# Kernel optimization log

Measured on AMD Instinct MI355X. Metric: run time of the kernel, lower is better.

Reference implementation:

```python
import jax, jax.numpy as jnp
import numpy as np

B, S, D, H, HD = 2, 4096, 1024, 16, 64   # batch, seq, hidden, heads, head_dim
BLOCK, W = 64, 8                          # block size, local window in blocks (512 tokens)
ROPE_BASE = 10000.0


def _rope_tables(seq_len, dim, dtype):
    inv_freq = 1.0 / (ROPE_BASE ** (jnp.arange(0, dim, 2, dtype=jnp.float32) / dim))
    t = jnp.arange(seq_len, dtype=jnp.float32)
    freqs = jnp.einsum('i,j->ij', t, inv_freq)          # [S, dim/2]
    emb = jnp.concatenate([freqs, freqs], axis=-1)       # [S, dim]
    return jnp.cos(emb).astype(dtype), jnp.sin(emb).astype(dtype)


def _rotate_half(x):
    x1, x2 = x[..., : x.shape[-1] // 2], x[..., x.shape[-1] // 2:]
    return jnp.concatenate([-x2, x1], axis=-1)


def _apply_rope(q, k, position_ids):
    # q, k: [B, H, S, HD]; position_ids: [B, S]
    cos_t, sin_t = _rope_tables(S, HD, q.dtype)
    cos = cos_t[position_ids][:, None, :, :]             # [B, 1, S, HD]
    sin = sin_t[position_ids][:, None, :, :]
    q_emb = q * cos + _rotate_half(q) * sin
    k_emb = k * cos + _rotate_half(k) * sin
    return q_emb, k_emb


def _block_sparse_attention(q, k, v):
    # Causal block-sparse (sliding window of W blocks), DeepSpeed-style layout.
    # q, k, v: [B, H, S, HD]
    nb = S // BLOCK
    scale = 1.0 / jnp.sqrt(jnp.asarray(HD, q.dtype))
    qb = q.reshape(B, H, nb, BLOCK, HD)
    kb = k.reshape(B, H, nb, BLOCK, HD)
    vb = v.reshape(B, H, nb, BLOCK, HD)
    # block-column indices attended by each block-row: i-W+1 .. i
    idx = jnp.arange(nb)[:, None] - jnp.arange(W - 1, -1, -1)[None, :]   # [nb, W]
    valid = idx >= 0
    idxc = jnp.clip(idx, 0, nb - 1)
    kg = kb[:, :, idxc]                                   # [B, H, nb, W, BLOCK, HD]
    vg = vb[:, :, idxc]
    scores = jnp.einsum('bhnqd,bhnwkd->bhnqwk', qb, kg) * scale  # [B,H,nb,BLOCK,W,BLOCK]
    # absolute positions for causal mask within the window
    qpos = (jnp.arange(nb) * BLOCK)[:, None, None, None] + jnp.arange(BLOCK)[None, :, None, None]  # [nb,BLOCK,1,1]
    kpos = (idxc * BLOCK)[:, None, :, None] + jnp.arange(BLOCK)[None, None, None, :]               # [nb,1,W,BLOCK]
    mask = (kpos <= qpos) & valid[:, None, :, None]       # [nb, BLOCK, W, BLOCK]
    neg = jnp.asarray(-1e9, scores.dtype)
    scores = jnp.where(mask[None, None], scores, neg)
    scores = scores.reshape(B, H, nb, BLOCK, W * BLOCK)
    probs = jax.nn.softmax(scores, axis=-1)
    out = jnp.einsum('bhnqk,bhnkd->bhnqd', probs, vg.reshape(B, H, nb, W * BLOCK, HD))
    return out.reshape(B, H, S, HD)


def setup_inputs() -> dict:
    key = jax.random.key(0)
    ks = jax.random.split(key, 5)
    hidden_states = jax.random.normal(ks[0], (B, S, D), dtype=jnp.float32)
    position_ids = jnp.tile(jnp.arange(S, dtype=jnp.int32)[None, :], (B, 1))
    w_init = lambda k: (jax.random.normal(k, (D, D), dtype=jnp.float32) * 0.02)
    return {
        'hidden_states': hidden_states,
        'position_ids': position_ids,
        'wq': w_init(ks[1]),  # stored [in, out]
        'wk': w_init(ks[2]),
        'wv': w_init(ks[3]),
        'wo': w_init(ks[4]),
    }


def reference(hidden_states, position_ids, wq, wk, wv, wo):
    q = jnp.einsum('bsd,de->bse', hidden_states, wq).reshape(B, S, H, HD).transpose(0, 2, 1, 3)
    k = jnp.einsum('bsd,de->bse', hidden_states, wk).reshape(B, S, H, HD).transpose(0, 2, 1, 3)
    v = jnp.einsum('bsd,de->bse', hidden_states, wv).reshape(B, S, H, HD).transpose(0, 2, 1, 3)
    q, k = _apply_rope(q, k, position_ids)
    attn = _block_sparse_attention(q, k, v)               # [B, H, S, HD]
    attn = attn.transpose(0, 2, 1, 3).reshape(B, S, D)
    return jnp.einsum('bsd,de->bse', attn, wo)
```

## Files before the change

### kernel.cpp

```cpp
#include <hip/hip_runtime.h>
#include <cstdint>
#include <cstddef>

#define B_ 2
#define S_ 4096
#define D_ 1024
#define H_ 16
#define HD_ 64
#define NB_ 64
#define W_ 8
#define M_ (B_*S_)

#define QSCALE 0.18033688011112042f
#define LOG2_10000_OVER_32 0.41524101186092034f

typedef __bf16 bf16_t;
typedef __bf16 bf16x8 __attribute__((ext_vector_type(8)));
typedef float f32x4 __attribute__((ext_vector_type(4)));

#define GLOAD_LDS16(gp, lp) \
  __builtin_amdgcn_global_load_lds((__attribute__((address_space(1))) void*)(gp), \
                                   (__attribute__((address_space(3))) void*)(lp), 16, 0, 0)
#define WAITV(n) asm volatile("s_waitcnt vmcnt(" #n ")" ::: "memory")
#define BAR() do { __builtin_amdgcn_s_barrier(); asm volatile("" ::: "memory"); } while (0)

__global__ __launch_bounds__(256) void prep_kernel(const float* __restrict__ hs,
                                                   bf16_t* __restrict__ hsb,
                                                   const float* __restrict__ w0,
                                                   const float* __restrict__ w1,
                                                   const float* __restrict__ w2,
                                                   const float* __restrict__ w3,
                                                   bf16_t* __restrict__ wT) {
  __shared__ float tile[32][33];
  const int bid = blockIdx.x;
  if (bid < (M_ * D_ / 4) / 256) {
    int i = bid * 256 + threadIdx.x;
    float4 v = ((const float4*)hs)[i];
    union { bf16_t b[4]; uint2 u; } cv;
    cv.b[0] = (bf16_t)v.x; cv.b[1] = (bf16_t)v.y; cv.b[2] = (bf16_t)v.z; cv.b[3] = (bf16_t)v.w;
    ((uint2*)hsb)[i] = cv.u;
  } else {
    const int b2 = bid - (M_ * D_ / 4) / 256;
    const int z = b2 >> 10;
    const int rem = b2 & 1023;
    const int bx = rem & 31, by = rem >> 5;
    const float* w = (z == 0) ? w0 : (z == 1) ? w1 : (z == 2) ? w2 : w3;
    bf16_t* wt = wT + (size_t)z * D_ * D_;
    const int tx = threadIdx.x & 31, ty = threadIdx.x >> 5;
    const int x = bx * 32 + tx;
    const int y0 = by * 32;
    for (int i = ty; i < 32; i += 8)
      tile[i][tx] = w[(size_t)(y0 + i) * D_ + x];
    __syncthreads();
    const int x2 = by * 32 + tx;
    const int y2 = bx * 32;
    for (int i = ty; i < 32; i += 8)
      wt[(size_t)(y2 + i) * D_ + x2] = (bf16_t)tile[tx][i];
  }
}

__global__ __launch_bounds__(512, 4) void gemm_qkv256(const bf16_t* __restrict__ A,
                                                      const bf16_t* __restrict__ Bt,
                                                      bf16_t* __restrict__ qkv,
                                                      bf16_t* __restrict__ vt_out,
                                                      const int* __restrict__ pos_ids) {
  const int bid = blockIdx.x;
  const int sid = (bid & 7) * 48 + (bid >> 3);
  const int mb = sid / 12, nb = sid % 12;
  const int mbase = mb * 256, nbase = nb * 256;
  const int tid = threadIdx.x;
  const int wid = tid >> 6, lane = tid & 63;
  const int quad = lane >> 4, l16 = lane & 15;
  const int wr = wid >> 2, wc = wid & 3;

  __shared__ bf16_t lds[3 * 16384];

  const int srow = wid * 16 + (lane >> 2);
  const int schunk = (lane & 3) ^ ((lane >> 3) & 3);
  const bf16_t* gAb = A  + (size_t)(mbase + srow) * D_ + schunk * 8;
  const bf16_t* gBb = Bt + (size_t)(nbase + srow) * D_ + schunk * 8;
  const int quadx = (quad ^ ((l16 >> 1) & 3)) * 8;

#define LDSA(b) (lds + (b) * 16384)
#define LDSB(b) (lds + (b) * 16384 + 8192)
#define STAGE(kt) do { bf16_t* pa_ = LDSA((kt) % 3) + wid * 512; \
    bf16_t* pb_ = LDSB((kt) % 3) + wid * 512; \
    GLOAD_LDS16(gAb + (kt) * 32, pa_); \
    GLOAD_LDS16(gAb + (size_t)128 * D_ + (kt) * 32, pa_ + 4096); \
    GLOAD_LDS16(gBb + (kt) * 32, pb_); \
    GLOAD_LDS16(gBb + (size_t)128 * D_ + (kt) * 32, pb_ + 4096); } while (0)

  f32x4 acc[8][4];
#pragma unroll
  for (int m = 0; m < 8; ++m)
#pragma unroll
    for (int n = 0; n < 4; ++n) acc[m][n] = (f32x4){0.f, 0.f, 0.f, 0.f};

#define PHASE(kt, STG, WT) do { \
    const bf16_t* Ab_ = LDSA((kt) % 3); \
    const bf16_t* Bb_ = LDSB((kt) % 3); \
    bf16x8 af_[8], bf_[4]; \
    _Pragma("unroll") \
    for (int m = 0; m < 8; ++m) \
      af_[m] = *(const bf16x8*)&Ab_[(wr * 128 + m * 16 + l16) * 32 + quadx]; \
    _Pragma("unroll") \
    for (int n = 0; n < 4; ++n) \
      bf_[n] = *(const bf16x8*)&Bb_[(wc * 64 + n * 16 + l16) * 32 + quadx]; \
    STG; \
    __builtin_amdgcn_s_setprio(1); \
    _Pragma("unroll") \
    for (int m = 0; m < 8; ++m) \
      _Pragma("unroll") \
      for (int n = 0; n < 4; ++n) \
        acc[m][n] = __builtin_amdgcn_mfma_f32_16x16x32_bf16(af_[m], bf_[n], acc[m][n], 0, 0, 0); \
    __builtin_amdgcn_s_setprio(0); \
    WT; \
    BAR(); \
  } while (0)

  STAGE(0); STAGE(1);
  WAITV(4);
  BAR();

#pragma unroll 3
  for (int kt = 0; kt < 30; ++kt)
    PHASE(kt, STAGE(kt + 2), WAITV(4));
  PHASE(30, (void)0, WAITV(0));
  PHASE(31, (void)0, (void)0);

  const int zsl = nb >> 2;
  if (zsl < 2) {
    bf16_t* Cp = qkv + (size_t)zsl * M_ * D_;
    const float qsc = (zsl == 0) ? QSCALE : 1.0f;
    float invf[2];
#pragma unroll
    for (int ni = 0; ni < 2; ++ni)
      invf[ni] = __builtin_exp2f(-(float)(ni * 16 + l16) * LOG2_10000_OVER_32);
    const int colb = (nb & 3) * 256 + wc * 64;
#pragma unroll
    for (int m = 0; m < 8; ++m) {
#pragma unroll
      for (int r = 0; r < 4; ++r) {
        int row = mbase + wr * 128 + m * 16 + quad * 4 + r;
        float fpos = (float)pos_ids[row];
#pragma unroll
        for (int ni = 0; ni < 2; ++ni) {
          float sn, cs;
          __sincosf(fpos * invf[ni], &sn, &cs);
          float x1 = acc[m][ni][r], x2 = acc[m][ni + 2][r];
          int col = colb + ni * 16 + l16;
          Cp[(size_t)row * D_ + col]      = (bf16_t)((x1 * cs - x2 * sn) * qsc);
          Cp[(size_t)row * D_ + col + 32] = (bf16_t)((x2 * cs + x1 * sn) * qsc);
        }
      }
    }
  } else {
    const int h = (nb & 3) * 4 + wc;
#pragma unroll
    for (int mh = 0; mh < 2; ++mh) {
      int rowblk = mb * 4 + wr * 2 + mh;
      int bb = rowblk >> 6, sblk = rowblk & 63;
      size_t vbase = (size_t)(bb * H_ + h) * HD_ * S_;
#pragma unroll
      for (int n = 0; n < 4; ++n) {
        int d = n * 16 + l16;
        union { bf16_t bv[16]; uint4 u[2]; } pk;
#pragma unroll
        for (int r = 0; r < 4; ++r)
#pragma unroll
          for (int mi = 0; mi < 4; ++mi)
            pk.bv[r * 4 + mi] = (bf16_t)acc[mh * 4 + mi][n][r];
        size_t addr = vbase + (size_t)d * S_ + (size_t)sblk * 64 + quad * 16;
        *(uint4*)&vt_out[addr]     = pk.u[0];
        *(uint4*)&vt_out[addr + 8] = pk.u[1];
      }
    }
  }
#undef PHASE
#undef STAGE
#undef LDSA
#undef LDSB
}

template<bool OBF>
__global__ __launch_bounds__(256) void gemm128(const bf16_t* __restrict__ A,
                                               const bf16_t* __restrict__ BtBase,
                                               void* __restrict__ Cbase,
                                               bf16_t* __restrict__ vt_out,
                                               const int* __restrict__ pos_ids) {
  const bf16_t* Bt = BtBase + (size_t)blockIdx.z * D_ * D_;
  const int mb = blockIdx.y * 128, nb = blockIdx.x * 128;
  const int tid = threadIdx.x;
  const int wid = tid >> 6, lane = tid & 63;
  const int quad = lane >> 4, l16 = lane & 15;
  const int wr = wid >> 1, wc = wid & 1;

  __shared__ bf16_t As[128 * 32];
  __shared__ bf16_t Bs[128 * 32];

  f32x4 acc[4][4];
#pragma unroll
  for (int mi = 0; mi < 4; ++mi)
#pragma unroll
    for (int ni = 0; ni < 4; ++ni)
      acc[mi][ni] = (f32x4){0.f, 0.f, 0.f, 0.f};

  const int acol = ((lane & 3) ^ ((lane >> 3) & 3)) * 8;
  const int arow0 = wid * 32 + (lane >> 2);
  const int quadx = (quad ^ ((l16 >> 1) & 3)) * 8;
  const bf16_t* gA = A + (size_t)(mb + arow0) * D_ + acol;
  const bf16_t* gB = Bt + (size_t)(nb + arow0) * D_ + acol;

  for (int kt = 0; kt < 32; ++kt) {
    const int k0 = kt * 32;
    __syncthreads();
#pragma unroll
    for (int c = 0; c < 2; ++c) {
      GLOAD_LDS16(gA + (size_t)c * 16 * D_ + k0, As + (wid * 2 + c) * 512);
      GLOAD_LDS16(gB + (size_t)c * 16 * D_ + k0, Bs + (wid * 2 + c) * 512);
    }
    __syncthreads();
    bf16x8 af[4], bfr[4];
#pragma unroll
    for (int mi = 0; mi < 4; ++mi)
      af[mi] = *(const bf16x8*)&As[(wr * 64 + mi * 16 + l16) * 32 + quadx];
#pragma unroll
    for (int ni = 0; ni < 4; ++ni)
      bfr[ni] = *(const bf16x8*)&Bs[(wc * 64 + ni * 16 + l16) * 32 + quadx];
#pragma unroll
    for (int mi = 0; mi < 4; ++mi)
#pragma unroll
      for (int ni = 0; ni < 4; ++ni)
        acc[mi][ni] = __builtin_amdgcn_mfma_f32_16x16x32_bf16(af[mi], bfr[ni], acc[mi][ni], 0, 0, 0);
  }

  if constexpr (OBF) {
  } else {
    float* Cp = (float*)Cbase;
#pragma unroll
    for (int mi = 0; mi < 4; ++mi)
#pragma unroll
      for (int ni = 0; ni < 4; ++ni)
#pragma unroll
        for (int r = 0; r < 4; ++r) {
          int row = mb + wr * 64 + mi * 16 + quad * 4 + r;
          int col = nb + wc * 64 + ni * 16 + l16;
          Cp[(size_t)row * D_ + col] = acc[mi][ni][r];
        }
  }
}

__global__ __launch_bounds__(256) void attn_kernel(const bf16_t* __restrict__ q,
                                                   const bf16_t* __restrict__ k,
                                                   const bf16_t* __restrict__ vt,
                                                   bf16_t* __restrict__ o) {
  const int m = blockIdx.x, h = blockIdx.y, b = blockIdx.z;
  const int n0 = m * 2, n1 = n0 + 1;
  const int tid = threadIdx.x;
  const int wid = tid >> 6, lane = tid & 63;
  const int quad = lane >> 4, l16 = lane & 15;

  __shared__ bf16_t Ks[2][64 * 64];
  __shared__ bf16_t Vs[2][64 * 64];
  __shared__ bf16_t Ps[4][16 * 72];

  const size_t hoff = (size_t)h * HD_;
  const size_t vtbase = (size_t)(b * H_ + h) * HD_ * S_;
  const size_t rowb[2] = {(size_t)(b * S_ + n0 * 64), (size_t)(b * S_ + n1 * 64)};

  bf16x8 aq[2][2];
#pragma unroll
  for (int x = 0; x < 2; ++x) {
    const bf16_t* qr = q + (rowb[x] + wid * 16 + l16) * D_ + hoff;
    aq[x][0] = *(const bf16x8*)(qr + quad * 8);
    aq[x][1] = *(const bf16x8*)(qr + 32 + quad * 8);
  }

  f32x4 o_acc[2][4];
  float lsum[2][4];
#pragma unroll
  for (int x = 0; x < 2; ++x)
#pragma unroll
    for (int t = 0; t < 4; ++t) {
      o_acc[x][t] = (f32x4){0.f, 0.f, 0.f, 0.f};
      lsum[x][t] = 0.f;
    }

  const int srK = wid * 16 + (lane >> 3);
  const int scC = ((lane & 7) ^ ((lane >> 3) & 7)) * 8;
  const bf16_t* kbase = k + (size_t)(b * S_) * D_ + hoff;
  const bf16_t* vbase2 = vt + vtbase;
#define STAGE_KV(kb_, buf_) do { \
    bf16_t* kd = &Ks[buf_][wid * 1024]; \
    bf16_t* vd = &Vs[buf_][wid * 1024]; \
    GLOAD_LDS16(kbase + (size_t)((kb_) * 64 + srK) * D_ + scC, kd); \
    GLOAD_LDS16(kbase + (size_t)((kb_) * 64 + srK + 8) * D_ + scC, kd + 512); \
    GLOAD_LDS16(vbase2 + (size_t)srK * S_ + (kb_) * 64 + scC, vd); \
    GLOAD_LDS16(vbase2 + (size_t)(srK + 8) * S_ + (kb_) * 64 + scC, vd + 512); \
  } while (0)

  const int ck0 = (quad ^ (l16 & 7)) * 8;
  const int ck1 = ((quad ^ 4) ^ (l16 & 7)) * 8;

  const int kb0 = (n0 >= W_ - 1) ? n0 - (W_ - 1) : 0;

  STAGE_KV(kb0, kb0 & 1);

  for (int kb = kb0; kb <= n1; ++kb) {
    const int buf = kb & 1;
    if (kb < n1) { STAGE_KV(kb + 1, buf ^ 1); WAITV(4); }
    else        { WAITV(0); }
    BAR();

#pragma unroll
    for (int x = 0; x < 2; ++x) {
      const int nx = n0 + x;
      if (x == 0 ? (kb > n0) : (kb < n1 - (W_ - 1))) continue;

      f32x4 sacc[4];
#pragma unroll
      for (int t = 0; t < 4; ++t) sacc[t] = (f32x4){0.f, 0.f, 0.f, 0.f};
#pragma unroll
      for (int t = 0; t < 4; ++t) {
        const int rr = (t * 16 + l16) * 64;
        bf16x8 bk0 = *(const bf16x8*)&Ks[buf][rr + ck0];
        bf16x8 bk1 = *(const bf16x8*)&Ks[buf][rr + ck1];
        sacc[t] = __builtin_amdgcn_mfma_f32_16x16x32_bf16(aq[x][0], bk0, sacc[t], 0, 0, 0);
        sacc[t] = __builtin_amdgcn_mfma_f32_16x16x32_bf16(aq[x][1], bk1, sacc[t], 0, 0, 0);
      }

      const bool diag = (kb == nx);
#pragma unroll
      for (int r = 0; r < 4; ++r) {
        int qpos = wid * 16 + quad * 4 + r;
        union { bf16_t bv[4]; uint2 u; } pk;
        float rs = 0.f;
#pragma unroll
        for (int t = 0; t < 4; ++t) {
          float p = __builtin_exp2f(sacc[t][r]);
          if (diag && (t * 16 + l16 > qpos)) p = 0.f;
          rs += p;
          pk.bv[t] = (bf16_t)p;
        }
        lsum[x][r] += rs;
        *(uint2*)&Ps[wid][(quad * 4 + r) * 72 + l16 * 4] = pk.u;
      }

      bf16x8 pa0 = *(const bf16x8*)&Ps[wid][l16 * 72 + quad * 8];
      bf16x8 pa1 = *(const bf16x8*)&Ps[wid][l16 * 72 + 32 + quad * 8];
#pragma unroll
      for (int t = 0; t < 4; ++t) {
        const int rr = (t * 16 + l16) * 64;
        bf16x8 vb0 = *(const bf16x8*)&Vs[buf][rr + ck0];
        bf16x8 vb1 = *(const bf16x8*)&Vs[buf][rr + ck1];
        o_acc[x][t] = __builtin_amdgcn_mfma_f32_16x16x32_bf16(pa0, vb0, o_acc[x][t], 0, 0, 0);
        o_acc[x][t] = __builtin_amdgcn_mfma_f32_16x16x32_bf16(pa1, vb1, o_acc[x][t], 0, 0, 0);
      }
    }
    BAR();
  }
#undef STAGE_KV

#pragma unroll
  for (int x = 0; x < 2; ++x) {
    float inv[4];
#pragma unroll
    for (int r = 0; r < 4; ++r) {
      float s = lsum[x][r];
#pragma unroll
      for (int off = 1; off < 16; off <<= 1) s += __shfl_xor(s, off);
      inv[r] = 1.f / s;
    }
#pragma unroll
    for (int t = 0; t < 4; ++t)
#pragma unroll
      for (int r = 0; r < 4; ++r) {
        int row = wid * 16 + quad * 4 + r;
        int col = t * 16 + l16;
        o[(rowb[x] + row) * D_ + hoff + col] = (bf16_t)(o_acc[x][t][r] * inv[r]);
      }
  }
}

extern "C" void kernel_launch(void* const* d_in, const int* in_sizes, int n_in,
                              void* d_out, int out_size, void* d_ws, size_t ws_size,
                              hipStream_t stream) {
  const float* hs = (const float*)d_in[0];
  const int* pos  = (const int*)d_in[1];
  const float* wq = (const float*)d_in[2];
  const float* wk = (const float*)d_in[3];
  const float* wv = (const float*)d_in[4];
  const float* wo = (const float*)d_in[5];

  bf16_t* ws   = (bf16_t*)d_ws;
  bf16_t* hsb  = ws;
  bf16_t* wT   = hsb + (size_t)M_ * D_;
  bf16_t* qkv  = wT + (size_t)4 * D_ * D_;
  bf16_t* attn = qkv + (size_t)3 * M_ * D_;
  bf16_t* qw  = qkv;
  bf16_t* kw  = qkv + (size_t)M_ * D_;
  bf16_t* vtg = qkv + (size_t)2 * M_ * D_;

  prep_kernel<<<dim3((M_ * D_ / 4) / 256 + 4 * 1024), 256, 0, stream>>>(hs, hsb, wq, wk, wv, wo, wT);
  gemm_qkv256<<<dim3(384), dim3(512), 0, stream>>>(hsb, wT, qkv, vtg, pos);
  attn_kernel<<<dim3(NB_ / 2, H_, B_), 256, 0, stream>>>(qw, kw, vtg, attn);
  gemm128<false><<<dim3(D_ / 128, M_ / 128, 1), 256, 0, stream>>>(attn, wT + (size_t)3 * D_ * D_, d_out, nullptr, pos);
}
```

Measured before the change: 239.7 us.

## Unify GEMMs into templated 128x256 pipelined kernel for QKV and output projection

Shrinks the QKV GEMM tile from 256x256 to 128x256, doubling the block count to 768 for better CU fill. It also replaces the simple single-buffered 128x128 output-projection GEMM with the same triple-buffered, direct-to-LDS pipelined kernel (256 blocks of 512 threads). The smaller QKV tile lowers per-block reuse, which raises global and L2 traffic per FLOP, and the output projection now has fewer, larger blocks.

Measured after the change: 221.8 us. 1.08x faster.

```diff
diff --git a/kernel.cpp b/kernel.cpp
--- a/kernel.cpp
+++ b/kernel.cpp
@@ -59,21 +59,22 @@
   }
 }
 
-__global__ __launch_bounds__(512, 4) void gemm_qkv256(const bf16_t* __restrict__ A,
-                                                      const bf16_t* __restrict__ Bt,
-                                                      bf16_t* __restrict__ qkv,
-                                                      bf16_t* __restrict__ vt_out,
-                                                      const int* __restrict__ pos_ids) {
+template<int NBC>
+__global__ __launch_bounds__(512, 4) void gemm_bk(const bf16_t* __restrict__ A,
+                                                  const bf16_t* __restrict__ Bt,
+                                                  void* __restrict__ Cbase,
+                                                  bf16_t* __restrict__ vt_out,
+                                                  const int* __restrict__ pos_ids) {
   const int bid = blockIdx.x;
-  const int sid = (bid & 7) * 48 + (bid >> 3);
-  const int mb = sid / 12, nb = sid % 12;
-  const int mbase = mb * 256, nbase = nb * 256;
+  const int sid = (bid & 7) * (NBC * 8) + (bid >> 3);
+  const int mb = sid / NBC, nb = sid % NBC;
+  const int mbase = mb * 128, nbase = nb * 256;
   const int tid = threadIdx.x;
   const int wid = tid >> 6, lane = tid & 63;
   const int quad = lane >> 4, l16 = lane & 15;
   const int wr = wid >> 2, wc = wid & 3;
 
-  __shared__ bf16_t lds[3 * 16384];
+  __shared__ bf16_t lds[3 * 12288];
 
   const int srow = wid * 16 + (lane >> 2);
   const int schunk = (lane & 3) ^ ((lane >> 3) & 3);
@@ -81,35 +82,33 @@
   const bf16_t* gBb = Bt + (size_t)(nbase + srow) * D_ + schunk * 8;
   const int quadx = (quad ^ ((l16 >> 1) & 3)) * 8;
 
-#define LDSA(b) (lds + (b) * 16384)
-#define LDSB(b) (lds + (b) * 16384 + 8192)
-#define STAGE(kt) do { bf16_t* pa_ = LDSA((kt) % 3) + wid * 512; \
-    bf16_t* pb_ = LDSB((kt) % 3) + wid * 512; \
+#define STAGE(kt) do { \
+    bf16_t* pa_ = lds + ((kt) % 3) * 12288 + wid * 512; \
+    bf16_t* pb_ = lds + ((kt) % 3) * 12288 + 4096 + wid * 512; \
     GLOAD_LDS16(gAb + (kt) * 32, pa_); \
-    GLOAD_LDS16(gAb + (size_t)128 * D_ + (kt) * 32, pa_ + 4096); \
     GLOAD_LDS16(gBb + (kt) * 32, pb_); \
     GLOAD_LDS16(gBb + (size_t)128 * D_ + (kt) * 32, pb_ + 4096); } while (0)
 
-  f32x4 acc[8][4];
-#pragma unroll
-  for (int m = 0; m < 8; ++m)
+  f32x4 acc[4][4];
+#pragma unroll
+  for (int m = 0; m < 4; ++m)
 #pragma unroll
     for (int n = 0; n < 4; ++n) acc[m][n] = (f32x4){0.f, 0.f, 0.f, 0.f};
 
 #define PHASE(kt, STG, WT) do { \
-    const bf16_t* Ab_ = LDSA((kt) % 3); \
-    const bf16_t* Bb_ = LDSB((kt) % 3); \
-    bf16x8 af_[8], bf_[4]; \
+    const bf16_t* Ab_ = lds + ((kt) % 3) * 12288; \
+    const bf16_t* Bb_ = Ab_ + 4096; \
+    bf16x8 af_[4], bf_[4]; \
     _Pragma("unroll") \
-    for (int m = 0; m < 8; ++m) \
-      af_[m] = *(const bf16x8*)&Ab_[(wr * 128 + m * 16 + l16) * 32 + quadx]; \
+    for (int m = 0; m < 4; ++m) \
+      af_[m] = *(const bf16x8*)&Ab_[(wr * 64 + m * 16 + l16) * 32 + quadx]; \
     _Pragma("unroll") \
     for (int n = 0; n < 4; ++n) \
       bf_[n] = *(const bf16x8*)&Bb_[(wc * 64 + n * 16 + l16) * 32 + quadx]; \
     STG; \
     __builtin_amdgcn_s_setprio(1); \
     _Pragma("unroll") \
-    for (int m = 0; m < 8; ++m) \
+    for (int m = 0; m < 4; ++m) \
       _Pragma("unroll") \
       for (int n = 0; n < 4; ++n) \
         acc[m][n] = __builtin_amdgcn_mfma_f32_16x16x32_bf16(af_[m], bf_[n], acc[m][n], 0, 0, 0); \
@@ -119,47 +118,46 @@
   } while (0)
 
   STAGE(0); STAGE(1);
-  WAITV(4);
+  WAITV(3);
   BAR();
 
 #pragma unroll 3
   for (int kt = 0; kt < 30; ++kt)
-    PHASE(kt, STAGE(kt + 2), WAITV(4));
+    PHASE(kt, STAGE(kt + 2), WAITV(3));
   PHASE(30, (void)0, WAITV(0));
   PHASE(31, (void)0, (void)0);
 
-  const int zsl = nb >> 2;
-  if (zsl < 2) {
-    bf16_t* Cp = qkv + (size_t)zsl * M_ * D_;
-    const float qsc = (zsl == 0) ? QSCALE : 1.0f;
-    float invf[2];
-#pragma unroll
-    for (int ni = 0; ni < 2; ++ni)
-      invf[ni] = __builtin_exp2f(-(float)(ni * 16 + l16) * LOG2_10000_OVER_32);
-    const int colb = (nb & 3) * 256 + wc * 64;
-#pragma unroll
-    for (int m = 0; m < 8; ++m) {
-#pragma unroll
-      for (int r = 0; r < 4; ++r) {
-        int row = mbase + wr * 128 + m * 16 + quad * 4 + r;
-        float fpos = (float)pos_ids[row];
-#pragma unroll
-        for (int ni = 0; ni < 2; ++ni) {
-          float sn, cs;
-          __sincosf(fpos * invf[ni], &sn, &cs);
-          float x1 = acc[m][ni][r], x2 = acc[m][ni + 2][r];
-          int col = colb + ni * 16 + l16;
-          Cp[(size_t)row * D_ + col]      = (bf16_t)((x1 * cs - x2 * sn) * qsc);
-          Cp[(size_t)row * D_ + col + 32] = (bf16_t)((x2 * cs + x1 * sn) * qsc);
+  if constexpr (NBC == 12) {
+    const int zsl = nb >> 2;
+    if (zsl < 2) {
+      bf16_t* Cp = (bf16_t*)Cbase + (size_t)zsl * M_ * D_;
+      const float qsc = (zsl == 0) ? QSCALE : 1.0f;
+      float invf[2];
+#pragma unroll
+      for (int ni = 0; ni < 2; ++ni)
+        invf[ni] = __builtin_exp2f(-(float)(ni * 16 + l16) * LOG2_10000_OVER_32);
+      const int colb = (nb & 3) * 256 + wc * 64;
+#pragma unroll
+      for (int m = 0; m < 4; ++m) {
+#pragma unroll
+        for (int r = 0; r < 4; ++r) {
+          int row = mbase + wr * 64 + m * 16 + quad * 4 + r;
+          float fpos = (float)pos_ids[row];
+#pragma unroll
+          for (int ni = 0; ni < 2; ++ni) {
+            float sn, cs;
+            __sincosf(fpos * invf[ni], &sn, &cs);
+            float x1 = acc[m][ni][r], x2 = acc[m][ni + 2][r];
+            int col = colb + ni * 16 + l16;
+            Cp[(size_t)row * D_ + col]      = (bf16_t)((x1 * cs - x2 * sn) * qsc);
+            Cp[(size_t)row * D_ + col + 32] = (bf16_t)((x2 * cs + x1 * sn) * qsc);
+          }
         }
       }
-    }
-  } else {
-    const int h = (nb & 3) * 4 + wc;
-#pragma unroll
-    for (int mh = 0; mh < 2; ++mh) {
-      int rowblk = mb * 4 + wr * 2 + mh;
-      int bb = rowblk >> 6, sblk = rowblk & 63;
+    } else {
+      const int h = (nb & 3) * 4 + wc;
+      const int g = mb * 2 + wr;
+      const int bb = g >> 6, sblk = g & 63;
       size_t vbase = (size_t)(bb * H_ + h) * HD_ * S_;
 #pragma unroll
       for (int n = 0; n < 4; ++n) {
@@ -169,85 +167,27 @@
         for (int r = 0; r < 4; ++r)
 #pragma unroll
           for (int mi = 0; mi < 4; ++mi)
-            pk.bv[r * 4 + mi] = (bf16_t)acc[mh * 4 + mi][n][r];
+            pk.bv[r * 4 + mi] = (bf16_t)acc[mi][n][r];
         size_t addr = vbase + (size_t)d * S_ + (size_t)sblk * 64 + quad * 16;
         *(uint4*)&vt_out[addr]     = pk.u[0];
         *(uint4*)&vt_out[addr + 8] = pk.u[1];
       }
     }
+  } else {
+    float* Cp = (float*)Cbase;
+#pragma unroll
+    for (int m = 0; m < 4; ++m)
+#pragma unroll
+      for (int n = 0; n < 4; ++n)
+#pragma unroll
+        for (int r = 0; r < 4; ++r) {
+          int row = mbase + wr * 64 + m * 16 + quad * 4 + r;
+          int col = nbase + wc * 64 + n * 16 + l16;
+          Cp[(size_t)row * D_ + col] = acc[m][n][r];
+        }
   }
 #undef PHASE
 #undef STAGE
-#undef LDSA
-#undef LDSB
-}
-
-template<bool OBF>
-__global__ __launch_bounds__(256) void gemm128(const bf16_t* __restrict__ A,
-                                               const bf16_t* __restrict__ BtBase,
-                                               void* __restrict__ Cbase,
-                                               bf16_t* __restrict__ vt_out,
-                                               const int* __restrict__ pos_ids) {
-  const bf16_t* Bt = BtBase + (size_t)blockIdx.z * D_ * D_;
-  const int mb = blockIdx.y * 128, nb = blockIdx.x * 128;
-  const int tid = threadIdx.x;
-  const int wid = tid >> 6, lane = tid & 63;
-  const int quad = lane >> 4, l16 = lane & 15;
-  const int wr = wid >> 1, wc = wid & 1;
-
-  __shared__ bf16_t As[128 * 32];
-  __shared__ bf16_t Bs[128 * 32];
-
-  f32x4 acc[4][4];
-#pragma unroll
-  for (int mi = 0; mi < 4; ++mi)
-#pragma unroll
-    for (int ni = 0; ni < 4; ++ni)
-      acc[mi][ni] = (f32x4){0.f, 0.f, 0.f, 0.f};
-
-  const int acol = ((lane & 3) ^ ((lane >> 3) & 3)) * 8;
-  const int arow0 = wid * 32 + (lane >> 2);
-  const int quadx = (quad ^ ((l16 >> 1) & 3)) * 8;
-  const bf16_t* gA = A + (size_t)(mb + arow0) * D_ + acol;
-  const bf16_t* gB = Bt + (size_t)(nb + arow0) * D_ + acol;
-
-  for (int kt = 0; kt < 32; ++kt) {
-    const int k0 = kt * 32;
-    __syncthreads();
-#pragma unroll
-    for (int c = 0; c < 2; ++c) {
-      GLOAD_LDS16(gA + (size_t)c * 16 * D_ + k0, As + (wid * 2 + c) * 512);
-      GLOAD_LDS16(gB + (size_t)c * 16 * D_ + k0, Bs + (wid * 2 + c) * 512);
-    }
-    __syncthreads();
-    bf16x8 af[4], bfr[4];
-#pragma unroll
-    for (int mi = 0; mi < 4; ++mi)
-      af[mi] = *(const bf16x8*)&As[(wr * 64 + mi * 16 + l16) * 32 + quadx];
-#pragma unroll
-    for (int ni = 0; ni < 4; ++ni)
-      bfr[ni] = *(const bf16x8*)&Bs[(wc * 64 + ni * 16 + l16) * 32 + quadx];
-#pragma unroll
-    for (int mi = 0; mi < 4; ++mi)
-#pragma unroll
-      for (int ni = 0; ni < 4; ++ni)
-        acc[mi][ni] = __builtin_amdgcn_mfma_f32_16x16x32_bf16(af[mi], bfr[ni], acc[mi][ni], 0, 0, 0);
-  }
-
-  if constexpr (OBF) {
-  } else {
-    float* Cp = (float*)Cbase;
-#pragma unroll
-    for (int mi = 0; mi < 4; ++mi)
-#pragma unroll
-      for (int ni = 0; ni < 4; ++ni)
-#pragma unroll
-        for (int r = 0; r < 4; ++r) {
-          int row = mb + wr * 64 + mi * 16 + quad * 4 + r;
-          int col = nb + wc * 64 + ni * 16 + l16;
-          Cp[(size_t)row * D_ + col] = acc[mi][ni][r];
-        }
-  }
 }
 
 __global__ __launch_bounds__(256) void attn_kernel(const bf16_t* __restrict__ q,
@@ -402,7 +342,7 @@
   bf16_t* vtg = qkv + (size_t)2 * M_ * D_;
 
   prep_kernel<<<dim3((M_ * D_ / 4) / 256 + 4 * 1024), 256, 0, stream>>>(hs, hsb, wq, wk, wv, wo, wT);
-  gemm_qkv256<<<dim3(384), dim3(512), 0, stream>>>(hsb, wT, qkv, vtg, pos);
+  gemm_bk<12><<<dim3(768), dim3(512), 0, stream>>>(hsb, wT, (void*)qkv, vtg, pos);
   attn_kernel<<<dim3(NB_ / 2, H_, B_), 256, 0, stream>>>(qw, kw, vtg, attn);
-  gemm128<false><<<dim3(D_ / 128, M_ / 128, 1), 256, 0, stream>>>(attn, wT + (size_t)3 * D_ * D_, d_out, nullptr, pos);
+  gemm_bk<4><<<dim3(256), dim3(512), 0, stream>>>(attn, wT + (size_t)3 * D_ * D_, d_out, nullptr, pos);
 }
```
